# Optimization experiments

Measured on AMD Instinct MI355X. Metric: run time of the kernel, lower is better.

The kernel has to match this reference:

```python
import jax, jax.numpy as jnp
import numpy as np

N, E, G, L, H, DIN = 50000, 800000, 500, 4, 64, 128
EPS = 1e-5


def _gcn(x, W, b, src, dst, n):
    h = x @ W
    loop = jnp.arange(n)
    s = jnp.concatenate([src, loop])
    d = jnp.concatenate([dst, loop])
    deg = jax.ops.segment_sum(jnp.ones(s.shape[0], x.dtype), d, num_segments=n)
    dinv = jax.lax.rsqrt(jnp.maximum(deg, 1.0))  # deg >= 1 due to self loops
    norm = (dinv[s] * dinv[d])[:, None]
    return jax.ops.segment_sum(h[s] * norm, d, num_segments=n) + b


def _g2(x, W, b, src, dst, n, p=2.0):
    # G2 gradient gate: tau = tanh(scatter_mean_over_src(|X_src - X_dst|^p))
    Xc = jax.nn.relu(_gcn(x, W, b, src, dst, n))
    diff = jnp.abs(Xc[src] - Xc[dst]) ** p  # [E, H]
    s = jax.ops.segment_sum(diff, src, num_segments=n)
    cnt = jax.ops.segment_sum(jnp.ones(src.shape[0], x.dtype), src, num_segments=n)
    return jnp.tanh(s / jnp.maximum(cnt, 1.0)[:, None])


def _bn(x, g, b):
    # BatchNorm1d with batch statistics (training-mode normalization)
    m = x.mean(0)
    v = x.var(0)
    return (x - m) * jax.lax.rsqrt(v + EPS) * g + b


def setup_inputs() -> dict:
    key = jax.random.key(0)
    ks = jax.random.split(key, 24)
    sc_in = 1.0 / np.sqrt(DIN)
    sc_h = 1.0 / np.sqrt(H)
    inp = {
        "x": jax.random.normal(ks[0], (N, DIN), jnp.float32),
        "edge_index": jax.random.randint(ks[1], (2, E), 0, N),
        "batch": jnp.sort(jax.random.randint(ks[2], (N,), 0, G)),
        "preW": jax.random.normal(ks[3], (DIN, H), jnp.float32) * sc_in,
        "preb": jnp.zeros((H,), jnp.float32),
        "convW": jax.random.normal(ks[4], (L, H, H), jnp.float32) * sc_h,
        "convb": jnp.zeros((L, H), jnp.float32),
        "ggW": jax.random.normal(ks[5], (L, H, H), jnp.float32) * sc_h,
        "ggb": jnp.zeros((L, H), jnp.float32),
        "lin1W": jax.random.normal(ks[6], (H, H), jnp.float32) * sc_h,
        "lin1b": jnp.zeros((H,), jnp.float32),
        "lin2W": jax.random.normal(ks[7], (H, H), jnp.float32) * sc_h,
        "lin2b": jnp.zeros((H,), jnp.float32),
        "lin3W": jax.random.normal(ks[8], (H, H), jnp.float32) * sc_h,
        "lin3b": jnp.zeros((H,), jnp.float32),
        "lin4W": jax.random.normal(ks[9], (H, 1), jnp.float32) * sc_h,
        "lin4b": jnp.zeros((1,), jnp.float32),
        "bn_g": jnp.ones((H,), jnp.float32),
        "bn_b": jnp.zeros((H,), jnp.float32),
    }
    return inp


def reference(x, edge_index, batch, preW, preb, convW, convb, ggW, ggb,
              lin1W, lin1b, lin2W, lin2b, lin3W, lin3b, lin4W, lin4b,
              bn_g, bn_b):
    src, dst = edge_index[0], edge_index[1]
    # prelinear (dropout disabled / eval)
    x = jax.nn.relu(x @ preW + preb)
    for l in range(L):
        x_ = jax.nn.relu(_gcn(x, convW[l], convb[l], src, dst, N))
        tau = _g2(x, ggW[l], ggb[l], src, dst, N)
        x = (1.0 - tau) * x + tau * x_
    # readout: global add pool per graph -> [G, H]
    h = jax.ops.segment_sum(x, batch, num_segments=G)
    out = jax.nn.relu(_bn(h @ lin1W + lin1b, bn_g, bn_b))
    out = jax.nn.relu(_bn(out @ lin2W + lin2b, bn_g, bn_b))
    out = jax.nn.relu(_bn(out @ lin3W + lin3b, bn_g, bn_b))
    out = out @ lin4W + lin4b  # [G, 1]
    energy = 0.5 * jnp.sum((x[src] - x[dst]) ** 2)  # dirichlet energy of final x
    return (out, out, energy)
```

## Files before the change

### kernel.cpp

```cpp
#include <hip/hip_runtime.h>
#include <hip/hip_bf16.h>


#define N_NODES 50000
#define N_EDGES 800000
#define N_GRAPH 500
#define N_LAYERS 4
#define HDIM 64
#define DDIN 128
#define BN_EPS 1e-5f
#define NEPART 256
#define SC_CHUNK 2048
#define SC_NBLK ((N_NODES + SC_CHUNK - 1) / SC_CHUNK)


__global__ __launch_bounds__(256) void k_degrees(const int* __restrict__ ei,
                                                 int* __restrict__ deg_in,
                                                 int* __restrict__ deg_out) {
  int e = blockIdx.x * 256 + threadIdx.x;
  if (e >= N_EDGES) return;
  int s = ei[e], d = ei[N_EDGES + e];
  atomicAdd(&deg_out[s], 1);
  atomicAdd(&deg_in[d], 1);
}

__global__ __launch_bounds__(256) void k_scan1(const int* __restrict__ deg_in,
                                               const int* __restrict__ deg_out,
                                               int* __restrict__ rp_dst,
                                               int* __restrict__ rp_src,
                                               int* __restrict__ bsum) {
  int arr = blockIdx.y;
  const int* in = arr ? deg_out : deg_in;
  int* out = arr ? rp_src : rp_dst;
  int base = blockIdx.x * SC_CHUNK + threadIdx.x * 8;
  int v[8];
  int s = 0;
#pragma unroll
  for (int j = 0; j < 8; ++j) {
    int ii = base + j;
    v[j] = (ii < N_NODES) ? in[ii] : 0;
    s += v[j];
  }
  __shared__ int sh[256];
  sh[threadIdx.x] = s;
  __syncthreads();
  for (int off = 1; off < 256; off <<= 1) {
    int t = (threadIdx.x >= off) ? sh[threadIdx.x - off] : 0;
    __syncthreads();
    sh[threadIdx.x] += t;
    __syncthreads();
  }
  int run = sh[threadIdx.x] - s;
#pragma unroll
  for (int j = 0; j < 8; ++j) {
    int ii = base + j;
    if (ii < N_NODES) out[ii] = run;
    run += v[j];
  }
  if (threadIdx.x == 255) bsum[arr * SC_NBLK + blockIdx.x] = sh[255];
}

__global__ __launch_bounds__(64) void k_scan2(const int* __restrict__ bsum,
                                              int* __restrict__ boff,
                                              int* __restrict__ rp_dst,
                                              int* __restrict__ rp_src) {
  int lane = threadIdx.x;
  for (int a = 0; a < 2; ++a) {
    int v = (lane < SC_NBLK) ? bsum[a * SC_NBLK + lane] : 0;
    int incl = v;
    for (int off = 1; off < 64; off <<= 1) {
      int t = __shfl_up(incl, off);
      if (lane >= off) incl += t;
    }
    if (lane < SC_NBLK) boff[a * SC_NBLK + lane] = incl - v;
  }
  if (lane == 0) {
    rp_dst[N_NODES] = N_EDGES;
    rp_src[N_NODES] = N_EDGES;
  }
}

__global__ __launch_bounds__(256) void k_scan3(const int* __restrict__ boff,
                                               int* __restrict__ rp_dst,
                                               int* __restrict__ rp_src,
                                               int* __restrict__ cur_dst,
                                               int* __restrict__ cur_src,
                                               const int* __restrict__ deg_in,
                                               float* __restrict__ dinv) {
  int arr = blockIdx.y;
  int* rp = arr ? rp_src : rp_dst;
  int* cur = arr ? cur_src : cur_dst;
  int off = boff[arr * SC_NBLK + blockIdx.x];
  int base = blockIdx.x * SC_CHUNK + threadIdx.x * 8;
#pragma unroll
  for (int j = 0; j < 8; ++j) {
    int ii = base + j;
    if (ii < N_NODES) {
      int v = rp[ii] + off;
      rp[ii] = v;
      cur[ii] = v;
      if (arr == 0) dinv[ii] = rsqrtf((float)(deg_in[ii] + 1));
    }
  }
}

__global__ __launch_bounds__(256) void k_fill(const int* __restrict__ ei,
                                              int* __restrict__ cur_dst,
                                              int* __restrict__ cur_src,
                                              int* __restrict__ csr_dst,
                                              int* __restrict__ csr_src) {
  int e = blockIdx.x * 256 + threadIdx.x;
  if (e >= N_EDGES) return;
  int s = ei[e], d = ei[N_EDGES + e];
  int p = atomicAdd(&cur_dst[d], 1);
  csr_dst[p] = s;
  int q = atomicAdd(&cur_src[s], 1);
  csr_src[q] = d;
}


__global__ __launch_bounds__(256) void k_prelin(const float* __restrict__ x0,
                                                const float* __restrict__ W,
                                                const float* __restrict__ b,
                                                float* __restrict__ x) {
  __shared__ float Ws[DDIN * HDIM];
  for (int t = threadIdx.x; t < DDIN * HDIM; t += 256) Ws[t] = W[t];
  __syncthreads();
  int wave = threadIdx.x >> 6, lane = threadIdx.x & 63;
  float bias = b[lane];
  int stride = gridDim.x * 4;
  for (int i = blockIdx.x * 4 + wave; i < N_NODES; i += stride) {
    const float* xr = x0 + (size_t)i * DDIN;
    float xl0 = xr[lane], xl1 = xr[64 + lane];
    float acc = bias;
#pragma unroll
    for (int k = 0; k < 64; ++k) acc = fmaf(__shfl(xl0, k), Ws[k * 64 + lane], acc);
#pragma unroll
    for (int k = 0; k < 64; ++k) acc = fmaf(__shfl(xl1, k), Ws[(64 + k) * 64 + lane], acc);
    x[(size_t)i * HDIM + lane] = fmaxf(acc, 0.f);
  }
}

__global__ __launch_bounds__(256) void k_agg_gemm(const float* __restrict__ x,
                                                  const int* __restrict__ rp,
                                                  const int* __restrict__ csr,
                                                  const float* __restrict__ dinv,
                                                  const float* __restrict__ W1,
                                                  const float* __restrict__ W2,
                                                  const float* __restrict__ b1,
                                                  const float* __restrict__ b2,
                                                  float* __restrict__ x_,
                                                  float* __restrict__ Xc) {
  __shared__ float W1s[HDIM * HDIM], W2s[HDIM * HDIM];
  for (int t = threadIdx.x; t < HDIM * HDIM; t += 256) {
    W1s[t] = W1[t];
    W2s[t] = W2[t];
  }
  __syncthreads();
  int wave = threadIdx.x >> 6, lane = threadIdx.x & 63;
  float bb1 = b1[lane], bb2 = b2[lane];
  int stride = gridDim.x * 4;
  for (int i = blockIdx.x * 4 + wave; i < N_NODES; i += stride) {
    int e0 = rp[i], e1 = rp[i + 1];
    float di = dinv[i];
    size_t li = (size_t)i * HDIM + lane;
    float a0 = x[li] * di, a1 = 0.f, a2 = 0.f, a3 = 0.f;
    for (int base = e0; base < e1; base += 64) {
      int m = e1 - base;
      if (m > 64) m = 64;
      int idx = csr[base + (lane < m ? lane : 0)];
      float dv = dinv[idx];
      int k = 0;
      for (; k + 8 <= m; k += 8) {
        int s0 = __shfl(idx, k), s1 = __shfl(idx, k + 1), s2 = __shfl(idx, k + 2),
            s3 = __shfl(idx, k + 3), s4 = __shfl(idx, k + 4), s5 = __shfl(idx, k + 5),
            s6 = __shfl(idx, k + 6), s7 = __shfl(idx, k + 7);
        float w0 = __shfl(dv, k), w1 = __shfl(dv, k + 1), w2 = __shfl(dv, k + 2),
              w3 = __shfl(dv, k + 3), w4 = __shfl(dv, k + 4), w5 = __shfl(dv, k + 5),
              w6 = __shfl(dv, k + 6), w7 = __shfl(dv, k + 7);
        float v0 = x[(size_t)s0 * HDIM + lane], v1 = x[(size_t)s1 * HDIM + lane];
        float v2 = x[(size_t)s2 * HDIM + lane], v3 = x[(size_t)s3 * HDIM + lane];
        float v4 = x[(size_t)s4 * HDIM + lane], v5 = x[(size_t)s5 * HDIM + lane];
        float v6 = x[(size_t)s6 * HDIM + lane], v7 = x[(size_t)s7 * HDIM + lane];
        a0 = fmaf(v0, w0, a0);
        a1 = fmaf(v1, w1, a1);
        a2 = fmaf(v2, w2, a2);
        a3 = fmaf(v3, w3, a3);
        a0 = fmaf(v4, w4, a0);
        a1 = fmaf(v5, w5, a1);
        a2 = fmaf(v6, w6, a2);
        a3 = fmaf(v7, w7, a3);
      }
      for (; k < m; ++k) {
        int s = __shfl(idx, k);
        float w = __shfl(dv, k);
        a0 = fmaf(x[(size_t)s * HDIM + lane], w, a0);
      }
    }
    float acc = (a0 + a1 + a2 + a3) * di;
    float r1 = 0.f, r2 = 0.f;
#pragma unroll
    for (int k = 0; k < 64; ++k) {
      float xv = __shfl(acc, k);
      r1 = fmaf(xv, W1s[k * 64 + lane], r1);
      r2 = fmaf(xv, W2s[k * 64 + lane], r2);
    }
    x_[li] = fmaxf(r1 + bb1, 0.f);
    Xc[li] = fmaxf(r2 + bb2, 0.f);
  }
}

__global__ __launch_bounds__(256) void k_gate(const float* __restrict__ Xc,
                                              const float* __restrict__ x_,
                                              const int* __restrict__ rp,
                                              const int* __restrict__ csr,
                                              float* __restrict__ x) {
  int i = (blockIdx.x * 256 + threadIdx.x) >> 6;
  int lane = threadIdx.x & 63;
  if (i >= N_NODES) return;
  int e0 = rp[i], e1 = rp[i + 1];
  float xi = Xc[(size_t)i * HDIM + lane];
  float a0 = 0.f, a1 = 0.f, a2 = 0.f, a3 = 0.f;
  for (int base = e0; base < e1; base += 64) {
    int m = e1 - base;
    if (m > 64) m = 64;
    int idx = csr[base + (lane < m ? lane : 0)];
    int k = 0;
    for (; k + 8 <= m; k += 8) {
      int s0 = __shfl(idx, k), s1 = __shfl(idx, k + 1), s2 = __shfl(idx, k + 2),
          s3 = __shfl(idx, k + 3), s4 = __shfl(idx, k + 4), s5 = __shfl(idx, k + 5),
          s6 = __shfl(idx, k + 6), s7 = __shfl(idx, k + 7);
      float v0 = Xc[(size_t)s0 * HDIM + lane], v1 = Xc[(size_t)s1 * HDIM + lane];
      float v2 = Xc[(size_t)s2 * HDIM + lane], v3 = Xc[(size_t)s3 * HDIM + lane];
      float v4 = Xc[(size_t)s4 * HDIM + lane], v5 = Xc[(size_t)s5 * HDIM + lane];
      float v6 = Xc[(size_t)s6 * HDIM + lane], v7 = Xc[(size_t)s7 * HDIM + lane];
      float t0 = xi - v0, t1 = xi - v1, t2 = xi - v2, t3 = xi - v3;
      float t4 = xi - v4, t5 = xi - v5, t6 = xi - v6, t7 = xi - v7;
      a0 = fmaf(t0, t0, a0);
      a1 = fmaf(t1, t1, a1);
      a2 = fmaf(t2, t2, a2);
      a3 = fmaf(t3, t3, a3);
      a0 = fmaf(t4, t4, a0);
      a1 = fmaf(t5, t5, a1);
      a2 = fmaf(t6, t6, a2);
      a3 = fmaf(t7, t7, a3);
    }
    for (; k < m; ++k) {
      int d = __shfl(idx, k);
      float t = xi - Xc[(size_t)d * HDIM + lane];
      a0 = fmaf(t, t, a0);
    }
  }
  int cnt = e1 - e0;
  float tau = tanhf((a0 + a1 + a2 + a3) / (float)(cnt > 0 ? cnt : 1));
  size_t idx = (size_t)i * HDIM + lane;
  x[idx] = (1.f - tau) * x[idx] + tau * x_[idx];
}

__global__ __launch_bounds__(256) void k_epool(const float* __restrict__ x,
                                               const int* __restrict__ rp,
                                               const int* __restrict__ csr,
                                               const int* __restrict__ batch,
                                               float* __restrict__ hpool,
                                               float* __restrict__ epart) {
  int i = (blockIdx.x * 256 + threadIdx.x) >> 6;
  int lane = threadIdx.x & 63;
  if (i >= N_NODES) return;
  float xi = x[(size_t)i * HDIM + lane];
  int e0 = rp[i], e1 = rp[i + 1];
  float a0 = 0.f, a1 = 0.f, a2 = 0.f, a3 = 0.f;
  for (int base = e0; base < e1; base += 64) {
    int m = e1 - base;
    if (m > 64) m = 64;
    int idx = csr[base + (lane < m ? lane : 0)];
    int k = 0;
    for (; k + 8 <= m; k += 8) {
      int s0 = __shfl(idx, k), s1 = __shfl(idx, k + 1), s2 = __shfl(idx, k + 2),
          s3 = __shfl(idx, k + 3), s4 = __shfl(idx, k + 4), s5 = __shfl(idx, k + 5),
          s6 = __shfl(idx, k + 6), s7 = __shfl(idx, k + 7);
      float v0 = x[(size_t)s0 * HDIM + lane], v1 = x[(size_t)s1 * HDIM + lane];
      float v2 = x[(size_t)s2 * HDIM + lane], v3 = x[(size_t)s3 * HDIM + lane];
      float v4 = x[(size_t)s4 * HDIM + lane], v5 = x[(size_t)s5 * HDIM + lane];
      float v6 = x[(size_t)s6 * HDIM + lane], v7 = x[(size_t)s7 * HDIM + lane];
      float t0 = xi - v0, t1 = xi - v1, t2 = xi - v2, t3 = xi - v3;
      float t4 = xi - v4, t5 = xi - v5, t6 = xi - v6, t7 = xi - v7;
      a0 = fmaf(t0, t0, a0);
      a1 = fmaf(t1, t1, a1);
      a2 = fmaf(t2, t2, a2);
      a3 = fmaf(t3, t3, a3);
      a0 = fmaf(t4, t4, a0);
      a1 = fmaf(t5, t5, a1);
      a2 = fmaf(t6, t6, a2);
      a3 = fmaf(t7, t7, a3);
    }
    for (; k < m; ++k) {
      int d = __shfl(idx, k);
      float t = xi - x[(size_t)d * HDIM + lane];
      a0 = fmaf(t, t, a0);
    }
  }
  int g = batch[i];
  atomicAdd(&hpool[g * HDIM + lane], xi);
  float acc = a0 + a1 + a2 + a3;
  acc += __shfl_down(acc, 32);
  acc += __shfl_down(acc, 16);
  acc += __shfl_down(acc, 8);
  acc += __shfl_down(acc, 4);
  acc += __shfl_down(acc, 2);
  acc += __shfl_down(acc, 1);
  if (lane == 0) atomicAdd(&epart[i & (NEPART - 1)], acc);
}

__global__ __launch_bounds__(256) void k_esum(const float* __restrict__ epart,
                                              float* __restrict__ out_e) {
  __shared__ float sh[NEPART];
  int t = threadIdx.x;
  sh[t] = epart[t];
  __syncthreads();
  for (int off = NEPART / 2; off > 0; off >>= 1) {
    if (t < off) sh[t] += sh[t + off];
    __syncthreads();
  }
  if (t == 0) out_e[0] = 0.5f * sh[0];
}


__global__ __launch_bounds__(64) void k_mlp(const float* __restrict__ Hin,
                                            const float* __restrict__ W,
                                            const float* __restrict__ b,
                                            float* __restrict__ Z) {
  int r = blockIdx.x, c = threadIdx.x;
  float xl = Hin[r * HDIM + c];
  float acc = b[c];
#pragma unroll
  for (int k = 0; k < 64; ++k) acc = fmaf(__shfl(xl, k), W[k * HDIM + c], acc);
  Z[r * HDIM + c] = acc;
}

__global__ __launch_bounds__(256) void k_bn(float* __restrict__ Z,
                                            const float* __restrict__ g,
                                            const float* __restrict__ b) {
  int c = blockIdx.x;
  int tid = threadIdx.x;
  __shared__ float red[256];
  float v0 = (tid < N_GRAPH) ? Z[tid * HDIM + c] : 0.f;
  float v1 = (tid + 256 < N_GRAPH) ? Z[(tid + 256) * HDIM + c] : 0.f;
  red[tid] = v0 + v1;
  __syncthreads();
  for (int off = 128; off > 0; off >>= 1) {
    if (tid < off) red[tid] += red[tid + off];
    __syncthreads();
  }
  float mean = red[0] / (float)N_GRAPH;
  __syncthreads();
  float d0 = (tid < N_GRAPH) ? v0 - mean : 0.f;
  float d1 = (tid + 256 < N_GRAPH) ? v1 - mean : 0.f;
  red[tid] = d0 * d0 + d1 * d1;
  __syncthreads();
  for (int off = 128; off > 0; off >>= 1) {
    if (tid < off) red[tid] += red[tid + off];
    __syncthreads();
  }
  float var = red[0] / (float)N_GRAPH;
  float scale = rsqrtf(var + BN_EPS) * g[c];
  float bias = b[c];
  if (tid < N_GRAPH) Z[tid * HDIM + c] = fmaxf(fmaf(d0, scale, bias), 0.f);
  if (tid + 256 < N_GRAPH) Z[(tid + 256) * HDIM + c] = fmaxf(fmaf(d1, scale, bias), 0.f);
}

__global__ __launch_bounds__(256) void k_final(const float* __restrict__ H,
                                               const float* __restrict__ w,
                                               const float* __restrict__ b,
                                               float* __restrict__ out) {
  int r = blockIdx.x * 256 + threadIdx.x;
  if (r >= N_GRAPH) return;
  float acc = b[0];
#pragma unroll
  for (int k = 0; k < 64; ++k) acc = fmaf(H[r * HDIM + k], w[k], acc);
  out[r] = acc;
  out[N_GRAPH + r] = acc;
}


extern "C" void kernel_launch(void* const* d_in, const int* in_sizes, int n_in,
                              void* d_out, int out_size, void* d_ws, size_t ws_size,
                              hipStream_t stream) {
  (void)in_sizes; (void)n_in; (void)out_size; (void)ws_size;
  const float* x0    = (const float*)d_in[0];
  const int*   ei    = (const int*)d_in[1];
  const int*   batch = (const int*)d_in[2];
  const float* preW  = (const float*)d_in[3];
  const float* preb  = (const float*)d_in[4];
  const float* convW = (const float*)d_in[5];
  const float* convb = (const float*)d_in[6];
  const float* ggW   = (const float*)d_in[7];
  const float* ggb   = (const float*)d_in[8];
  const float* lin1W = (const float*)d_in[9];
  const float* lin1b = (const float*)d_in[10];
  const float* lin2W = (const float*)d_in[11];
  const float* lin2b = (const float*)d_in[12];
  const float* lin3W = (const float*)d_in[13];
  const float* lin3b = (const float*)d_in[14];
  const float* lin4W = (const float*)d_in[15];
  const float* lin4b = (const float*)d_in[16];
  const float* bng   = (const float*)d_in[17];
  const float* bnb   = (const float*)d_in[18];
  float* out = (float*)d_out;

  char* ws = (char*)d_ws;
  size_t off = 0;
  auto alloc = [&](size_t bytes) -> void* {
    off = (off + 255) & ~(size_t)255;
    void* p = ws + off;
    off += bytes;
    return p;
  };
  int* deg_in   = (int*)alloc(2ull * N_NODES * 4);
  int* deg_out  = deg_in + N_NODES;
  int* rp_dst   = (int*)alloc((N_NODES + 1) * 4);
  int* rp_src   = (int*)alloc((N_NODES + 1) * 4);
  int* cur_dst  = (int*)alloc((N_NODES + 1) * 4);
  int* cur_src  = (int*)alloc((N_NODES + 1) * 4);
  int* bsum     = (int*)alloc(2 * SC_NBLK * 4);
  int* boff     = (int*)alloc(2 * SC_NBLK * 4);
  int* csr_dst  = (int*)alloc((size_t)N_EDGES * 4);
  int* csr_src  = (int*)alloc((size_t)N_EDGES * 4);
  float* dinv   = (float*)alloc(N_NODES * 4);
  float* x      = (float*)alloc((size_t)N_NODES * HDIM * 4);
  float* x_     = (float*)alloc((size_t)N_NODES * HDIM * 4);
  float* Xc     = (float*)alloc((size_t)N_NODES * HDIM * 4);
  float* hpool  = (float*)alloc(N_GRAPH * HDIM * 4);
  float* epart  = (float*)alloc(NEPART * 4);
  float* mlpA   = (float*)alloc(N_GRAPH * HDIM * 4);
  float* mlpB   = (float*)alloc(N_GRAPH * HDIM * 4);

  hipMemsetAsync(deg_in, 0, 2ull * N_NODES * 4, stream);
  hipMemsetAsync(hpool, 0, N_GRAPH * HDIM * 4, stream);
  hipMemsetAsync(epart, 0, NEPART * 4, stream);

  k_degrees<<<(N_EDGES + 255) / 256, 256, 0, stream>>>(ei, deg_in, deg_out);
  {
    dim3 g(SC_NBLK, 2);
    k_scan1<<<g, 256, 0, stream>>>(deg_in, deg_out, rp_dst, rp_src, bsum);
    k_scan2<<<1, 64, 0, stream>>>(bsum, boff, rp_dst, rp_src);
    k_scan3<<<g, 256, 0, stream>>>(boff, rp_dst, rp_src, cur_dst, cur_src, deg_in, dinv);
  }
  k_fill<<<(N_EDGES + 255) / 256, 256, 0, stream>>>(ei, cur_dst, cur_src, csr_dst, csr_src);

  k_prelin<<<512, 256, 0, stream>>>(x0, preW, preb, x);

  const int gnode = (N_NODES + 3) / 4;
  for (int l = 0; l < N_LAYERS; ++l) {
    k_agg_gemm<<<1024, 256, 0, stream>>>(x, rp_dst, csr_dst, dinv,
                                         convW + l * HDIM * HDIM, ggW + l * HDIM * HDIM,
                                         convb + l * HDIM, ggb + l * HDIM, x_, Xc);
    k_gate<<<gnode, 256, 0, stream>>>(Xc, x_, rp_src, csr_src, x);
  }

  k_epool<<<gnode, 256, 0, stream>>>(x, rp_src, csr_src, batch, hpool, epart);
  k_esum<<<1, NEPART, 0, stream>>>(epart, out + 2 * N_GRAPH);

  k_mlp<<<N_GRAPH, 64, 0, stream>>>(hpool, lin1W, lin1b, mlpA);
  k_bn<<<HDIM, 256, 0, stream>>>(mlpA, bng, bnb);
  k_mlp<<<N_GRAPH, 64, 0, stream>>>(mlpA, lin2W, lin2b, mlpB);
  k_bn<<<HDIM, 256, 0, stream>>>(mlpB, bng, bnb);
  k_mlp<<<N_GRAPH, 64, 0, stream>>>(mlpB, lin3W, lin3b, mlpA);
  k_bn<<<HDIM, 256, 0, stream>>>(mlpA, bng, bnb);
  k_final<<<(N_GRAPH + 255) / 256, 256, 0, stream>>>(mlpA, lin4W, lin4b, out);
}
```

Before: 1.024 ms.

## Partition CSR build atomics by node range and fuse MLP with batchnorm

Degree counting and CSR fill now run as grid-stride loops over 8 node-range partitions. Each block only performs atomics for endpoints in its partition, which localizes atomic traffic and improves L2 locality at the cost of every partition rereading the full edge list. Separately, each MLP layer's linear step is fused into the batchnorm kernel. Each block computes one output column for all graphs, which removes three launches and the intermediate round-trip but uses a strided per-row read of the hidden state.

New measurement: 981.9 us. 1.04x faster.

```diff
diff --git a/kernel.cpp b/kernel.cpp
--- a/kernel.cpp
+++ b/kernel.cpp
@@ -12,16 +12,24 @@
 #define NEPART 256
 #define SC_CHUNK 2048
 #define SC_NBLK ((N_NODES + SC_CHUNK - 1) / SC_CHUNK)
+#define NPARTS 8
+#define PRNG (N_NODES / NPARTS)
+#define FILL_BPP 56
 
 
 __global__ __launch_bounds__(256) void k_degrees(const int* __restrict__ ei,
                                                  int* __restrict__ deg_in,
                                                  int* __restrict__ deg_out) {
-  int e = blockIdx.x * 256 + threadIdx.x;
-  if (e >= N_EDGES) return;
-  int s = ei[e], d = ei[N_EDGES + e];
-  atomicAdd(&deg_out[s], 1);
-  atomicAdd(&deg_in[d], 1);
+  int part = blockIdx.x & (NPARTS - 1);
+  int slice = blockIdx.x >> 3;
+  int nslice = gridDim.x >> 3;
+  int lo = part * PRNG, hi = lo + PRNG;
+  int stride = nslice * 256;
+  for (int e = slice * 256 + threadIdx.x; e < N_EDGES; e += stride) {
+    int s = ei[e], d = ei[N_EDGES + e];
+    if (s >= lo && s < hi) atomicAdd(&deg_out[s], 1);
+    if (d >= lo && d < hi) atomicAdd(&deg_in[d], 1);
+  }
 }
 
 __global__ __launch_bounds__(256) void k_scan1(const int* __restrict__ deg_in,
@@ -109,13 +117,22 @@
                                               int* __restrict__ cur_src,
                                               int* __restrict__ csr_dst,
                                               int* __restrict__ csr_src) {
-  int e = blockIdx.x * 256 + threadIdx.x;
-  if (e >= N_EDGES) return;
-  int s = ei[e], d = ei[N_EDGES + e];
-  int p = atomicAdd(&cur_dst[d], 1);
-  csr_dst[p] = s;
-  int q = atomicAdd(&cur_src[s], 1);
-  csr_src[q] = d;
+  int part = blockIdx.x & (NPARTS - 1);
+  int slice = blockIdx.x >> 3;
+  int nslice = gridDim.x >> 3;
+  int lo = part * PRNG, hi = lo + PRNG;
+  int stride = nslice * 256;
+  for (int e = slice * 256 + threadIdx.x; e < N_EDGES; e += stride) {
+    int s = ei[e], d = ei[N_EDGES + e];
+    if (d >= lo && d < hi) {
+      int q = atomicAdd(&cur_dst[d], 1);
+      csr_dst[q] = s;
+    }
+    if (s >= lo && s < hi) {
+      int q = atomicAdd(&cur_src[s], 1);
+      csr_src[q] = d;
+    }
+  }
 }
 
 
@@ -325,47 +342,51 @@
 }
 
 
-__global__ __launch_bounds__(64) void k_mlp(const float* __restrict__ Hin,
-                                            const float* __restrict__ W,
-                                            const float* __restrict__ b,
-                                            float* __restrict__ Z) {
-  int r = blockIdx.x, c = threadIdx.x;
-  float xl = Hin[r * HDIM + c];
-  float acc = b[c];
-#pragma unroll
-  for (int k = 0; k < 64; ++k) acc = fmaf(__shfl(xl, k), W[k * HDIM + c], acc);
-  Z[r * HDIM + c] = acc;
-}
-
-__global__ __launch_bounds__(256) void k_bn(float* __restrict__ Z,
-                                            const float* __restrict__ g,
-                                            const float* __restrict__ b) {
+__global__ __launch_bounds__(256) void k_mlpbn(const float* __restrict__ Hin,
+                                               const float* __restrict__ W,
+                                               const float* __restrict__ b,
+                                               const float* __restrict__ g,
+                                               const float* __restrict__ bb,
+                                               float* __restrict__ Z) {
   int c = blockIdx.x;
-  int tid = threadIdx.x;
+  __shared__ float Wc[HDIM];
   __shared__ float red[256];
-  float v0 = (tid < N_GRAPH) ? Z[tid * HDIM + c] : 0.f;
-  float v1 = (tid + 256 < N_GRAPH) ? Z[(tid + 256) * HDIM + c] : 0.f;
-  red[tid] = v0 + v1;
+  if (threadIdx.x < HDIM) Wc[threadIdx.x] = W[threadIdx.x * HDIM + c];
+  __syncthreads();
+  int r0 = threadIdx.x, r1 = threadIdx.x + 256;
+  float bc = b[c];
+  float d0 = bc, d1 = bc;
+  if (r0 < N_GRAPH) {
+    const float* h = Hin + (size_t)r0 * HDIM;
+#pragma unroll
+    for (int k = 0; k < HDIM; ++k) d0 = fmaf(h[k], Wc[k], d0);
+  }
+  if (r1 < N_GRAPH) {
+    const float* h = Hin + (size_t)r1 * HDIM;
+#pragma unroll
+    for (int k = 0; k < HDIM; ++k) d1 = fmaf(h[k], Wc[k], d1);
+  }
+  red[threadIdx.x] = (r0 < N_GRAPH ? d0 : 0.f) + (r1 < N_GRAPH ? d1 : 0.f);
   __syncthreads();
   for (int off = 128; off > 0; off >>= 1) {
-    if (tid < off) red[tid] += red[tid + off];
+    if (threadIdx.x < off) red[threadIdx.x] += red[threadIdx.x + off];
     __syncthreads();
   }
   float mean = red[0] / (float)N_GRAPH;
   __syncthreads();
-  float d0 = (tid < N_GRAPH) ? v0 - mean : 0.f;
-  float d1 = (tid + 256 < N_GRAPH) ? v1 - mean : 0.f;
-  red[tid] = d0 * d0 + d1 * d1;
+  float t0 = (r0 < N_GRAPH) ? d0 - mean : 0.f;
+  float t1 = (r1 < N_GRAPH) ? d1 - mean : 0.f;
+  red[threadIdx.x] = t0 * t0 + t1 * t1;
   __syncthreads();
   for (int off = 128; off > 0; off >>= 1) {
-    if (tid < off) red[tid] += red[tid + off];
+    if (threadIdx.x < off) red[threadIdx.x] += red[threadIdx.x + off];
     __syncthreads();
   }
   float var = red[0] / (float)N_GRAPH;
   float scale = rsqrtf(var + BN_EPS) * g[c];
-  float bias = b[c];
-  if (tid < N_GRAPH) Z[tid * HDIM + c] = fmaxf(fmaf(d0, scale, bias), 0.f);
-  if (tid + 256 < N_GRAPH) Z[(tid + 256) * HDIM + c] = fmaxf(fmaf(d1, scale, bias), 0.f);
+  float bias = bb[c];
+  if (r0 < N_GRAPH) Z[(size_t)r0 * HDIM + c] = fmaxf(fmaf(t0, scale, bias), 0.f);
+  if (r1 < N_GRAPH) Z[(size_t)r1 * HDIM + c] = fmaxf(fmaf(t1, scale, bias), 0.f);
 }
 
 __global__ __launch_bounds__(256) void k_final(const float* __restrict__ H,
@@ -438,14 +459,14 @@
   hipMemsetAsync(hpool, 0, N_GRAPH * HDIM * 4, stream);
   hipMemsetAsync(epart, 0, NEPART * 4, stream);
 
-  k_degrees<<<(N_EDGES + 255) / 256, 256, 0, stream>>>(ei, deg_in, deg_out);
+  k_degrees<<<NPARTS * FILL_BPP, 256, 0, stream>>>(ei, deg_in, deg_out);
   {
     dim3 g(SC_NBLK, 2);
     k_scan1<<<g, 256, 0, stream>>>(deg_in, deg_out, rp_dst, rp_src, bsum);
     k_scan2<<<1, 64, 0, stream>>>(bsum, boff, rp_dst, rp_src);
     k_scan3<<<g, 256, 0, stream>>>(boff, rp_dst, rp_src, cur_dst, cur_src, deg_in, dinv);
   }
-  k_fill<<<(N_EDGES + 255) / 256, 256, 0, stream>>>(ei, cur_dst, cur_src, csr_dst, csr_src);
+  k_fill<<<NPARTS * FILL_BPP, 256, 0, stream>>>(ei, cur_dst, cur_src, csr_dst, csr_src);
 
   k_prelin<<<512, 256, 0, stream>>>(x0, preW, preb, x);
 
@@ -460,11 +481,8 @@
   k_epool<<<gnode, 256, 0, stream>>>(x, rp_src, csr_src, batch, hpool, epart);
   k_esum<<<1, NEPART, 0, stream>>>(epart, out + 2 * N_GRAPH);
 
-  k_mlp<<<N_GRAPH, 64, 0, stream>>>(hpool, lin1W, lin1b, mlpA);
-  k_bn<<<HDIM, 256, 0, stream>>>(mlpA, bng, bnb);
-  k_mlp<<<N_GRAPH, 64, 0, stream>>>(mlpA, lin2W, lin2b, mlpB);
-  k_bn<<<HDIM, 256, 0, stream>>>(mlpB, bng, bnb);
-  k_mlp<<<N_GRAPH, 64, 0, stream>>>(mlpB, lin3W, lin3b, mlpA);
-  k_bn<<<HDIM, 256, 0, stream>>>(mlpA, bng, bnb);
+  k_mlpbn<<<HDIM, 256, 0, stream>>>(hpool, lin1W, lin1b, bng, bnb, mlpA);
+  k_mlpbn<<<HDIM, 256, 0, stream>>>(mlpA, lin2W, lin2b, bng, bnb, mlpB);
+  k_mlpbn<<<HDIM, 256, 0, stream>>>(mlpB, lin3W, lin3b, bng, bnb, mlpA);
   k_final<<<(N_GRAPH + 255) / 256, 256, 0, stream>>>(mlpA, lin4W, lin4b, out);
 }
```
